# Kernel optimization log

Measured on AMD Instinct MI355X. Metric: run time of the kernel, lower is better.

## Reference

```python
import jax, jax.numpy as jnp
import numpy as np

B, N, M, DIN, H = 8, 2048, 2048, 512, 256
SCALE = float(np.sqrt(H))


def _lin_params(key, din, dout):
    kw, kb = jax.random.split(key)
    lim = 1.0 / np.sqrt(din)
    W = jax.random.uniform(kw, (din, dout), jnp.float32, -lim, lim)
    b = jax.random.uniform(kb, (dout,), jnp.float32, -lim, lim)
    return W, b


def setup_inputs() -> dict:
    key = jax.random.key(0)
    ks = jax.random.split(key, 16)
    inp = {
        "q_fp": jax.random.normal(ks[0], (B, N, DIN), jnp.float32),
        "v_ret": jax.random.normal(ks[1], (B, M, DIN), jnp.float32),
        "pi_star": jax.random.uniform(ks[2], (B, N, M), jnp.float32),
    }
    names = ["qs", "ks", "vs", "qe", "ke", "ve"]
    for i, nm in enumerate(names):
        W, b = _lin_params(ks[3 + i], DIN, H)
        inp[f"W{nm}"], inp[f"b{nm}"] = W, b
    inp["W1"], inp["b1"] = _lin_params(ks[10], 4 * H, H)
    inp["W2"], inp["b2"] = _lin_params(ks[11], H, H)
    inp["gamma"] = jnp.ones((1,), jnp.float32)
    inp["ew"] = jnp.array(1.0, jnp.float32)
    return inp


def _forward(q_fp, v_ret, pi_star, Wqs, bqs, Wks, bks, Wvs, bvs,
             Wqe, bqe, Wke, bke, Wve, bve, W1, b1, W2, b2, gamma, ew):
    q_struct = q_fp @ Wqs + bqs          # [B,N,H]
    k_struct = v_ret @ Wks + bks         # [B,M,H]
    v_struct = v_ret @ Wvs + bvs
    q_elec = q_fp @ Wqe + bqe
    k_elec = v_ret @ Wke + bke
    v_elec = v_ret @ Wve + bve

    structural_logits = jnp.einsum("bnh,bmh->bnm", q_struct, k_struct) / SCALE

    # cdist(p=2) via the quadratic expansion, clamped for numeric safety
    q2 = jnp.sum(q_elec * q_elec, -1, keepdims=True)          # [B,N,1]
    k2 = jnp.sum(k_elec * k_elec, -1, keepdims=True)          # [B,M,1]
    d2 = q2 + jnp.swapaxes(k2, -2, -1) - 2.0 * jnp.einsum("bnh,bmh->bnm", q_elec, k_elec)
    electronic_distance = jnp.sqrt(jnp.maximum(d2, 1e-12))    # [B,N,M]
    electronic_scale = jnp.maximum(
        electronic_distance.mean(axis=(-2, -1), keepdims=True), 1e-4)
    electronic_logits = -(electronic_distance / electronic_scale)

    pi_mask = gamma * jnp.log(jnp.maximum(pi_star, 1e-9))
    final_logits = structural_logits + ew * electronic_logits + pi_mask
    attn = jax.nn.softmax(final_logits, axis=-1)              # [B,N,M]

    ctx_s = jnp.einsum("bnm,bmh->bnh", attn, v_struct)
    ctx_e = jnp.einsum("bnm,bmh->bnh", attn, v_elec)
    fused = jnp.concatenate([ctx_s, ctx_e, ctx_s - ctx_e, ctx_s * ctx_e], axis=-1)
    h = jax.nn.silu(fused @ W1 + b1)
    return h @ W2 + b2


def reference(q_fp, v_ret, pi_star, Wqs, bqs, Wks, bks, Wvs, bvs,
              Wqe, bqe, Wke, bke, Wve, bve, W1, b1, W2, b2, gamma, ew):
    return _forward(q_fp, v_ret, pi_star, Wqs, bqs, Wks, bks, Wvs, bvs,
                    Wqe, bqe, Wke, bke, Wve, bve, W1, b1, W2, b2, gamma, ew)
```

## Files before the change

### kernel.cpp

```cpp
#include <hip/hip_runtime.h>

#define Bsz 8
#define Nq  2048
#define Mk  2048
#define BKt 32
#define BUFE (128 * BKt)

typedef __attribute__((ext_vector_type(8))) short   short8;
typedef __attribute__((ext_vector_type(4))) float   floatx4;

__device__ __forceinline__ unsigned short f2bf(float f) {
  union { float f; unsigned u; } x; x.f = f;
  unsigned r = x.u + 0x7fffu + ((x.u >> 16) & 1u);
  return (unsigned short)(r >> 16);
}
__device__ __forceinline__ float bf2f(unsigned short s) {
  union { unsigned u; float f; } x; x.u = ((unsigned)s) << 16;
  return x.f;
}

__device__ __forceinline__ void gload16(const unsigned short* g, unsigned short* l) {
  __builtin_amdgcn_global_load_lds(
      (const __attribute__((address_space(1))) void*)g,
      (__attribute__((address_space(3))) void*)l, 16, 0, 0);
}

__device__ __forceinline__ void gemm_core8_nt(
    const unsigned short* __restrict__ A, int lda,
    const unsigned short* __restrict__ B, int ldb,
    int K, unsigned short* ldsA, unsigned short* ldsB,
    floatx4 (&acc)[4][2])
{
  const int tid  = threadIdx.x;
  const int lane = tid & 63;
  const int wid  = tid >> 6;
  const int wm   = wid & 1;
  const int wn   = wid >> 1;
  const int fr   = lane & 15;
  const int fk   = (lane >> 4) << 3;
  const int lr   = lane >> 2;
  const int lc   = (lane & 3) << 3;
  const int r0   = wid << 4;

  const unsigned short* gA = A + (size_t)(r0 + lr) * lda + lc;
  const unsigned short* gB = B + (size_t)(r0 + lr) * ldb + lc;
  unsigned short* lA = ldsA + r0 * BKt;
  unsigned short* lB = ldsB + r0 * BKt;
  const unsigned short* fa = ldsA + (wm * 64 + fr) * BKt + fk;
  const unsigned short* fb = ldsB + (wn * 32 + fr) * BKt + fk;

  gload16(gA, lA); gA += BKt;
  gload16(gB, lB); gB += BKt;
  __syncthreads();

  int cur = 0;
  for (int k0 = 0; k0 < K; k0 += BKt) {
    const int nxt = cur ^ 1;
    if (k0 + BKt < K) {
      gload16(gA, lA + nxt * BUFE); gA += BKt;
      gload16(gB, lB + nxt * BUFE); gB += BKt;
    }
    const unsigned short* fac = fa + cur * BUFE;
    const unsigned short* fbc = fb + cur * BUFE;
    short8 af[4], bfr[2];
#pragma unroll
    for (int i = 0; i < 4; i++) af[i]  = *(const short8*)(fac + i * 16 * BKt);
#pragma unroll
    for (int j = 0; j < 2; j++) bfr[j] = *(const short8*)(fbc + j * 16 * BKt);
#pragma unroll
    for (int i = 0; i < 4; i++)
#pragma unroll
      for (int j = 0; j < 2; j++)
        acc[i][j] = __builtin_amdgcn_mfma_f32_16x16x32_bf16(af[i], bfr[j], acc[i][j], 0, 0, 0);
    __syncthreads();
    cur = nxt;
  }
}

#define EPILOGUE_VARS \
  const int lane = threadIdx.x & 63; \
  const int wid  = threadIdx.x >> 6; \
  const int wm   = wid & 1; \
  const int wn   = wid >> 1; \
  const int r4   = (lane >> 4) * 4;  \
  const int cn   = lane & 15; \
  (void)wid;

template<int MODE>
__global__ __launch_bounds__(512, 4) void k_gemm_bias(
    const unsigned short* __restrict__ A, const unsigned short* __restrict__ Bw,
    const float* __restrict__ bias, void* __restrict__ Cout, int Ncols, int K)
{
  __shared__ alignas(16) unsigned short ldsA[2 * BUFE];
  __shared__ alignas(16) unsigned short ldsB[2 * BUFE];
  floatx4 acc[4][2];
#pragma unroll
  for (int i = 0; i < 4; i++)
#pragma unroll
    for (int j = 0; j < 2; j++)
#pragma unroll
      for (int t = 0; t < 4; t++) acc[i][j][t] = 0.f;

  const unsigned short* Ab = A + (size_t)blockIdx.x * 128 * K;
  const unsigned short* Bb = Bw + (size_t)blockIdx.y * 128 * K;
  gemm_core8_nt(Ab, K, Bb, K, K, ldsA, ldsB, acc);

  EPILOGUE_VARS
#pragma unroll
  for (int i = 0; i < 4; i++) {
#pragma unroll
    for (int j = 0; j < 2; j++) {
      int gc = blockIdx.y * 128 + wn * 32 + j * 16 + cn;
      float bv = bias[gc];
#pragma unroll
      for (int r = 0; r < 4; r++) {
        int gr = blockIdx.x * 128 + wm * 64 + i * 16 + r4 + r;
        float v = acc[i][j][r] + bv;
        if constexpr (MODE == 1) v = v / (1.f + __expf(-v));
        if constexpr (MODE == 2)
          ((float*)Cout)[(size_t)gr * Ncols + gc] = v;
        else
          ((unsigned short*)Cout)[(size_t)gr * Ncols + gc] = f2bf(v);
      }
    }
  }
}

__global__ __launch_bounds__(512) void k_cast(
    const float* __restrict__ src, unsigned short* __restrict__ dst, int n8)
{
  for (int i = blockIdx.x * 512 + threadIdx.x; i < n8; i += gridDim.x * 512) {
    const float4 f0 = *(const float4*)(src + (size_t)i * 8);
    const float4 f1 = *(const float4*)(src + (size_t)i * 8 + 4);
    uint4 p;
    p.x = f2bf(f0.x) | ((unsigned)f2bf(f0.y) << 16);
    p.y = f2bf(f0.z) | ((unsigned)f2bf(f0.w) << 16);
    p.z = f2bf(f1.x) | ((unsigned)f2bf(f1.y) << 16);
    p.w = f2bf(f1.z) | ((unsigned)f2bf(f1.w) << 16);
    *(uint4*)(dst + (size_t)i * 8) = p;
  }
}

__global__ __launch_bounds__(512, 4) void k_sd(
    const unsigned short* __restrict__ Xq, const unsigned short* __restrict__ Xk,
    const float* __restrict__ q2, const float* __restrict__ k2,
    int b0, float* __restrict__ dsum, unsigned* __restrict__ sd)
{
  __shared__ alignas(16) unsigned short ldsAs[2 * BUFE];
  __shared__ alignas(16) unsigned short ldsAe[2 * BUFE];
  __shared__ alignas(16) unsigned short ldsBs[2 * BUFE];
  __shared__ alignas(16) unsigned short ldsBe[2 * BUFE];
  floatx4 accS[4][2], accE[4][2];
#pragma unroll
  for (int i = 0; i < 4; i++)
#pragma unroll
    for (int j = 0; j < 2; j++)
#pragma unroll
      for (int t = 0; t < 4; t++) { accS[i][j][t] = 0.f; accE[i][j][t] = 0.f; }

  const int z = blockIdx.z;
  const int b = b0 + z;

  const int tid  = threadIdx.x;
  const int lane = tid & 63;
  const int wid  = tid >> 6;
  const int wm   = wid & 1;
  const int wn   = wid >> 1;
  const int fr   = lane & 15;
  const int fk   = (lane >> 4) << 3;
  const int lr   = lane >> 2;
  const int lc   = (lane & 3) << 3;
  const int r0   = wid << 4;

  const unsigned short* gAs = Xq + ((size_t)(b * Nq) + blockIdx.x * 128 + r0 + lr) * 512 + lc;
  const unsigned short* gAe = gAs + 256;
  const unsigned short* gBs = Xk + ((size_t)(b * Mk) + blockIdx.y * 128 + r0 + lr) * 1024 + lc;
  const unsigned short* gBe = gBs + 512;
  unsigned short* lAs = ldsAs + r0 * BKt;
  unsigned short* lAe = ldsAe + r0 * BKt;
  unsigned short* lBs = ldsBs + r0 * BKt;
  unsigned short* lBe = ldsBe + r0 * BKt;
  const unsigned short* fas = ldsAs + (wm * 64 + fr) * BKt + fk;
  const unsigned short* fae = ldsAe + (wm * 64 + fr) * BKt + fk;
  const unsigned short* fbs = ldsBs + (wn * 32 + fr) * BKt + fk;
  const unsigned short* fbe = ldsBe + (wn * 32 + fr) * BKt + fk;

  gload16(gAs, lAs); gAs += BKt;
  gload16(gAe, lAe); gAe += BKt;
  gload16(gBs, lBs); gBs += BKt;
  gload16(gBe, lBe); gBe += BKt;
  __syncthreads();

  int cur = 0;
  for (int k0 = 0; k0 < 256; k0 += BKt) {
    const int nxt = cur ^ 1;
    if (k0 + BKt < 256) {
      gload16(gAs, lAs + nxt * BUFE); gAs += BKt;
      gload16(gAe, lAe + nxt * BUFE); gAe += BKt;
      gload16(gBs, lBs + nxt * BUFE); gBs += BKt;
      gload16(gBe, lBe + nxt * BUFE); gBe += BKt;
    }
    {
      short8 af[4], bfr[2];
      const unsigned short* fac = fas + cur * BUFE;
      const unsigned short* fbc = fbs + cur * BUFE;
#pragma unroll
      for (int i = 0; i < 4; i++) af[i]  = *(const short8*)(fac + i * 16 * BKt);
#pragma unroll
      for (int j = 0; j < 2; j++) bfr[j] = *(const short8*)(fbc + j * 16 * BKt);
#pragma unroll
      for (int i = 0; i < 4; i++)
#pragma unroll
        for (int j = 0; j < 2; j++)
          accS[i][j] = __builtin_amdgcn_mfma_f32_16x16x32_bf16(af[i], bfr[j], accS[i][j], 0, 0, 0);
    }
    {
      short8 af[4], bfr[2];
      const unsigned short* fac = fae + cur * BUFE;
      const unsigned short* fbc = fbe + cur * BUFE;
#pragma unroll
      for (int i = 0; i < 4; i++) af[i]  = *(const short8*)(fac + i * 16 * BKt);
#pragma unroll
      for (int j = 0; j < 2; j++) bfr[j] = *(const short8*)(fbc + j * 16 * BKt);
#pragma unroll
      for (int i = 0; i < 4; i++)
#pragma unroll
        for (int j = 0; j < 2; j++)
          accE[i][j] = __builtin_amdgcn_mfma_f32_16x16x32_bf16(af[i], bfr[j], accE[i][j], 0, 0, 0);
    }
    __syncthreads();
    cur = nxt;
  }

  const int r4 = (lane >> 4) * 4;
  const int cn = lane & 15;
  const int colT = blockIdx.y * 128 + wn * 32;
  const float kk0 = k2[b * Mk + colT + cn];
  const float kk1 = k2[b * Mk + colT + 16 + cn];

  float lsum = 0.f;
#pragma unroll
  for (int i = 0; i < 4; i++) {
#pragma unroll
    for (int r = 0; r < 4; r++) {
      const int n = blockIdx.x * 128 + wm * 64 + i * 16 + r4 + r;
      const float qq = q2[b * Nq + n];
      unsigned* srow = sd + (size_t)(z * Nq + n) * Mk;
#pragma unroll
      for (int j = 0; j < 2; j++) {
        const int m = colT + j * 16 + cn;
        float d = sqrtf(fmaxf(qq + (j ? kk1 : kk0) - 2.f * accE[i][j][r], 1e-12f));
        lsum += d;
        srow[m] = (unsigned)f2bf(accS[i][j][r] * 0.0625f)
                | ((unsigned)f2bf(d) << 16);
      }
    }
  }
#pragma unroll
  for (int o = 32; o; o >>= 1) lsum += __shfl_down(lsum, o);
  __syncthreads();
  float* red = (float*)ldsAs;
  if (lane == 0) red[wid] = lsum;
  __syncthreads();
  if (threadIdx.x == 0) {
    float s = 0.f;
#pragma unroll
    for (int t = 0; t < 8; t++) s += red[t];
    atomicAdd(dsum + b, s);
  }
}

__global__ __launch_bounds__(256) void k_softmax(
    const unsigned* __restrict__ sd, const float* __restrict__ pi,
    const float* __restrict__ dsum, const float* __restrict__ gamma_p,
    const float* __restrict__ ew_p, int b0,
    unsigned short* __restrict__ attn, float* __restrict__ rowsum)
{
  const int wid  = threadIdx.x >> 6;
  const int lane = threadIdx.x & 63;
  const int rl   = blockIdx.x * 4 + wid;
  const int b    = b0 + (rl >> 11);
  const int n    = rl & 2047;

  const float scale = fmaxf(dsum[b] * (1.f / (2048.f * 2048.f)), 1e-4f);
  const float einv  = ew_p[0] / scale;
  const float gv    = gamma_p[0];
  const bool  g1    = (gv == 1.0f);

  const unsigned*  sp = sd  + (size_t)rl * Mk;
  const float*     pp = pi  + ((size_t)b * Nq + n) * Mk;
  unsigned short*  ap = attn + ((size_t)b * Nq + n) * Mk;

  float rs = 0.f;
  for (int it = 0; it < 8; ++it) {
    const int c = it * 256 + lane * 4;
    const uint4  sv = *(const uint4*)(sp + c);
    const float4 pv = *(const float4*)(pp + c);
    const unsigned uu[4]  = {sv.x, sv.y, sv.z, sv.w};
    const float    pp4[4] = {pv.x, pv.y, pv.z, pv.w};
    float e[4];
#pragma unroll
    for (int t = 0; t < 4; ++t) {
      union { unsigned u; float f; } cs, cd;
      cs.u = uu[t] << 16;
      cd.u = uu[t] & 0xffff0000u;
      float p  = fmaxf(pp4[t], 1e-9f);
      float pf = g1 ? p : __expf(gv * __logf(p));
      e[t] = __expf(cs.f - einv * cd.f) * pf;
      rs += e[t];
    }
    uint2 st;
    st.x = (unsigned)f2bf(e[0]) | ((unsigned)f2bf(e[1]) << 16);
    st.y = (unsigned)f2bf(e[2]) | ((unsigned)f2bf(e[3]) << 16);
    *(uint2*)(ap + c) = st;
  }
#pragma unroll
  for (int o = 32; o; o >>= 1) rs += __shfl_down(rs, o);
  if (lane == 0) rowsum[b * Nq + n] = rs;
}

__global__ __launch_bounds__(512, 4) void k_pv(
    const unsigned short* __restrict__ At, const unsigned short* __restrict__ VT,
    const float* __restrict__ rowsum, unsigned short* __restrict__ ctx)
{
  __shared__ alignas(16) unsigned short ldsA[2 * BUFE];
  __shared__ alignas(16) unsigned short ldsB[2 * BUFE];
  floatx4 acc[4][2];
#pragma unroll
  for (int i = 0; i < 4; i++)
#pragma unroll
    for (int j = 0; j < 2; j++)
#pragma unroll
      for (int t = 0; t < 4; t++) acc[i][j][t] = 0.f;

  const int l  = blockIdx.x;
  const int lg = ((l & 7) << 3) | (l >> 3);
  const int tx = lg >> 2;
  const int ty = lg & 3;
  const int b  = blockIdx.z;
  const unsigned short* Ab = At + ((size_t)b * Nq + tx * 128) * (size_t)Mk;
  const unsigned short* Bb = VT + ((size_t)b * 512 + ty * 128) * (size_t)Mk;
  gemm_core8_nt(Ab, Mk, Bb, Mk, Mk, ldsA, ldsB, acc);

  EPILOGUE_VARS
  const int rowbase = b * Nq + tx * 128 + wm * 64;
#pragma unroll
  for (int i = 0; i < 4; i++) {
    float rinv[4];
#pragma unroll
    for (int r = 0; r < 4; r++)
      rinv[r] = 1.f / rowsum[rowbase + i * 16 + r4 + r];
#pragma unroll
    for (int j = 0; j < 2; j++) {
      int gc = ty * 128 + wn * 32 + j * 16 + cn;
#pragma unroll
      for (int r = 0; r < 4; r++) {
        int gr = tx * 128 + wm * 64 + i * 16 + r4 + r;
        ctx[((size_t)b * Nq + gr) * 512 + gc] = f2bf(acc[i][j][r] * rinv[r]);
      }
    }
  }
}

__global__ void k_prep_w(
    const float* __restrict__ Wqs, const float* __restrict__ Wqe,
    const float* __restrict__ Wks, const float* __restrict__ Wvs,
    const float* __restrict__ Wke, const float* __restrict__ Wve,
    const float* __restrict__ W1,  const float* __restrict__ W2,
    const float* __restrict__ bqs, const float* __restrict__ bqe,
    const float* __restrict__ bks, const float* __restrict__ bvs,
    const float* __restrict__ bke, const float* __restrict__ bve,
    unsigned short* __restrict__ WqT, unsigned short* __restrict__ WkT,
    unsigned short* __restrict__ W1T, unsigned short* __restrict__ W2T,
    float* __restrict__ bq, float* __restrict__ bk, float* __restrict__ dsum)
{
  int gid = blockIdx.x * 256 + threadIdx.x;
  int idx = gid;
  if (idx < 512 * 512) {
    int j = idx >> 9, k = idx & 511;
    float v = (j < 256) ? Wqs[k * 256 + j] : Wqe[k * 256 + (j - 256)];
    WqT[idx] = f2bf(v);
  } else if ((idx -= 512 * 512) < 1024 * 512) {
    int j = idx >> 9, k = idx & 511;
    int s = j >> 8, jj = j & 255;
    const float* Wp = (s == 0) ? Wks : (s == 1) ? Wvs : (s == 2) ? Wke : Wve;
    WkT[idx] = f2bf(Wp[k * 256 + jj]);
  } else if ((idx -= 1024 * 512) < 256 * 1024) {
    int j = idx >> 10, k = idx & 1023;
    W1T[idx] = f2bf(W1[k * 256 + j]);
  } else if ((idx -= 256 * 1024) < 256 * 256) {
    int j = idx >> 8, k = idx & 255;
    W2T[idx] = f2bf(W2[k * 256 + j]);
  }
  if (gid < 512)  bq[gid] = (gid < 256) ? bqs[gid] : bqe[gid - 256];
  if (gid < 1024) bk[gid] = (gid < 256) ? bks[gid]
                    : (gid < 512) ? bvs[gid - 256]
                    : (gid < 768) ? bke[gid - 512] : bve[gid - 768];
  if (gid < 8) dsum[gid] = 0.f;
}

__global__ __launch_bounds__(256) void k_rowsq(
    const unsigned short* __restrict__ X, int stride, int colOff, float* __restrict__ out)
{
  int row = blockIdx.x * 4 + (threadIdx.x >> 6);
  int lane = threadIdx.x & 63;
  const unsigned short* p = X + (size_t)row * stride + colOff + lane * 4;
  uint2 u = *(const uint2*)p;
  float a0 = bf2f((unsigned short)(u.x & 0xffff));
  float a1 = bf2f((unsigned short)(u.x >> 16));
  float a2 = bf2f((unsigned short)(u.y & 0xffff));
  float a3 = bf2f((unsigned short)(u.y >> 16));
  float s = a0 * a0 + a1 * a1 + a2 * a2 + a3 * a3;
#pragma unroll
  for (int o = 32; o; o >>= 1) s += __shfl_down(s, o);
  if (lane == 0) out[row] = s;
}

__global__ void k_trans_vt(const unsigned short* __restrict__ Xk, unsigned short* __restrict__ VT) {
  __shared__ unsigned short t[32][33];
  const int b = blockIdx.z;
  const int m0 = blockIdx.x * 32, j0 = blockIdx.y * 32;
  const int tx = threadIdx.x, ty = threadIdx.y;
#pragma unroll
  for (int i = 0; i < 4; i++) {
    int m = m0 + ty + i * 8;
    int j = j0 + tx;
    int c = (j < 256) ? (256 + j) : (512 + j);
    t[ty + i * 8][tx] = Xk[((size_t)b * Mk + m) * 1024 + c];
  }
  __syncthreads();
#pragma unroll
  for (int i = 0; i < 4; i++) {
    int j = j0 + ty + i * 8;
    int m = m0 + tx;
    VT[((size_t)b * 512 + j) * Mk + m] = t[tx][ty + i * 8];
  }
}

__global__ void k_fused(const unsigned short* __restrict__ ctx, unsigned short* __restrict__ fused) {
  int idx = blockIdx.x * 256 + threadIdx.x;
  int bn = idx >> 8;
  int j = idx & 255;
  float cs = bf2f(ctx[(size_t)bn * 512 + j]);
  float ce = bf2f(ctx[(size_t)bn * 512 + 256 + j]);
  size_t o = (size_t)bn * 1024 + j;
  fused[o]       = f2bf(cs);
  fused[o + 256] = f2bf(ce);
  fused[o + 512] = f2bf(cs - ce);
  fused[o + 768] = f2bf(cs * ce);
}

extern "C" void kernel_launch(void* const* d_in, const int* in_sizes, int n_in,
                              void* d_out, int out_size, void* d_ws, size_t ws_size,
                              hipStream_t stream) {
  (void)in_sizes; (void)n_in; (void)out_size; (void)ws_size;
  const float* q_fp  = (const float*)d_in[0];
  const float* v_ret = (const float*)d_in[1];
  const float* pi    = (const float*)d_in[2];
  const float* Wqs = (const float*)d_in[3];  const float* bqs = (const float*)d_in[4];
  const float* Wks = (const float*)d_in[5];  const float* bks = (const float*)d_in[6];
  const float* Wvs = (const float*)d_in[7];  const float* bvs = (const float*)d_in[8];
  const float* Wqe = (const float*)d_in[9];  const float* bqe = (const float*)d_in[10];
  const float* Wke = (const float*)d_in[11]; const float* bke = (const float*)d_in[12];
  const float* Wve = (const float*)d_in[13]; const float* bve = (const float*)d_in[14];
  const float* W1  = (const float*)d_in[15]; const float* b1  = (const float*)d_in[16];
  const float* W2  = (const float*)d_in[17]; const float* b2  = (const float*)d_in[18];
  const float* gamma = (const float*)d_in[19];
  const float* ew    = (const float*)d_in[20];

  char* w = (char*)d_ws;
  unsigned short* WqT = (unsigned short*)(w + 0);
  unsigned short* WkT = (unsigned short*)(w + 524288);
  unsigned short* W1T = (unsigned short*)(w + 1572864);
  unsigned short* W2T = (unsigned short*)(w + 2097152);
  float* bq   = (float*)(w + 2228224);
  float* bk   = (float*)(w + 2230272);
  float* q2   = (float*)(w + 2234368);
  float* k2   = (float*)(w + 2299904);
  float* dsum = (float*)(w + 2365440);
  unsigned short* ctx  = (unsigned short*)(w + 2365696);
  unsigned short* hbuf = (unsigned short*)(w + 19142912);
  unsigned short* Xq = (unsigned short*)(w + 35920128);
  unsigned short* Xk = (unsigned short*)(w + 52697344);
  unsigned short* VT = (unsigned short*)(w + 86251776);
  unsigned short* attn = (unsigned short*)(w + 103028992);
  unsigned short* fused = attn;
  unsigned short* castQ = (unsigned short*)(w + 103028992);
  unsigned short* castK = (unsigned short*)(w + 103028992 + 16777216);
  unsigned* sdbuf = (unsigned*)(w + 2365696);
  float* rowsum = (float*)d_out;

  k_prep_w<<<4352, 256, 0, stream>>>(Wqs, Wqe, Wks, Wvs, Wke, Wve, W1, W2,
                                     bqs, bqe, bks, bvs, bke, bve,
                                     WqT, WkT, W1T, W2T, bq, bk, dsum);
  k_cast<<<2048, 512, 0, stream>>>(q_fp,  castQ, (16384 * 512) / 8);
  k_cast<<<2048, 512, 0, stream>>>(v_ret, castK, (16384 * 512) / 8);
  k_gemm_bias<0><<<dim3(128, 4), 512, 0, stream>>>(castQ, WqT, bq, Xq, 512, 512);
  k_gemm_bias<0><<<dim3(128, 8), 512, 0, stream>>>(castK, WkT, bk, Xk, 1024, 512);
  k_rowsq<<<4096, 256, 0, stream>>>(Xq, 512, 256, q2);
  k_rowsq<<<4096, 256, 0, stream>>>(Xk, 1024, 512, k2);
  for (int c = 0; c < 4; ++c) {
    k_sd<<<dim3(16, 16, 2), 512, 0, stream>>>(Xq, Xk, q2, k2, 2 * c, dsum, sdbuf);
    k_softmax<<<1024, 256, 0, stream>>>(sdbuf, pi, dsum, gamma, ew, 2 * c,
                                        attn, rowsum);
  }
  k_trans_vt<<<dim3(64, 16, 8), dim3(32, 8), 0, stream>>>(Xk, VT);
  k_pv<<<dim3(64, 1, 8), 512, 0, stream>>>(attn, VT, rowsum, ctx);
  k_fused<<<16384, 256, 0, stream>>>(ctx, fused);
  k_gemm_bias<1><<<dim3(128, 2), 512, 0, stream>>>(fused, W1T, b1, hbuf, 256, 1024);
  k_gemm_bias<2><<<dim3(128, 2), 512, 0, stream>>>(hbuf, W2T, b2, d_out, 256, 256);
}
```

Baseline: 559.4 us.

## Fuse row-norms into projection GEMMs and fused-concat into PV epilogue

Folds the squared-norm reductions into the projection GEMM epilogues via shuffles and atomics, merges the two cast kernels, and has the PV kernel pair struct/elec column tiles per block so it writes the concatenated fused tensor directly. This removes several small launches and the intermediate ctx round trip through memory. In exchange it adds atomics with nondeterministic summation order, zero-init in prep, an LDS staging pass, and a workspace reshuffle where attn, hbuf and cast buffers alias.

```diff
diff --git a/kernel.cpp b/kernel.cpp
--- a/kernel.cpp
+++ b/kernel.cpp
@@ -126,18 +126,78 @@
   }
 }
 
-__global__ __launch_bounds__(512) void k_cast(
-    const float* __restrict__ src, unsigned short* __restrict__ dst, int n8)
-{
-  for (int i = blockIdx.x * 512 + threadIdx.x; i < n8; i += gridDim.x * 512) {
-    const float4 f0 = *(const float4*)(src + (size_t)i * 8);
-    const float4 f1 = *(const float4*)(src + (size_t)i * 8 + 4);
+__global__ __launch_bounds__(512, 4) void k_proj_sq(
+    const unsigned short* __restrict__ A, const unsigned short* __restrict__ Bw,
+    const float* __restrict__ bias, unsigned short* __restrict__ Cout,
+    int Ncols, int K, float* __restrict__ sq, int elecOff)
+{
+  __shared__ alignas(16) unsigned short ldsA[2 * BUFE];
+  __shared__ alignas(16) unsigned short ldsB[2 * BUFE];
+  floatx4 acc[4][2];
+#pragma unroll
+  for (int i = 0; i < 4; i++)
+#pragma unroll
+    for (int j = 0; j < 2; j++)
+#pragma unroll
+      for (int t = 0; t < 4; t++) acc[i][j][t] = 0.f;
+
+  const unsigned short* Ab = A + (size_t)blockIdx.x * 128 * K;
+  const unsigned short* Bb = Bw + (size_t)blockIdx.y * 128 * K;
+  gemm_core8_nt(Ab, K, Bb, K, K, ldsA, ldsB, acc);
+
+  EPILOGUE_VARS
+  const int c0 = blockIdx.y * 128;
+  const bool insq = (c0 >= elecOff) && (c0 < elecOff + 256);
+#pragma unroll
+  for (int i = 0; i < 4; i++) {
+    float s4[4] = {0.f, 0.f, 0.f, 0.f};
+#pragma unroll
+    for (int j = 0; j < 2; j++) {
+      int gc = c0 + wn * 32 + j * 16 + cn;
+      float bv = bias[gc];
+#pragma unroll
+      for (int r = 0; r < 4; r++) {
+        int gr = blockIdx.x * 128 + wm * 64 + i * 16 + r4 + r;
+        float v = acc[i][j][r] + bv;
+        unsigned short us = f2bf(v);
+        Cout[(size_t)gr * Ncols + gc] = us;
+        if (insq) { float vr = bf2f(us); s4[r] += vr * vr; }
+      }
+    }
+    if (insq) {
+#pragma unroll
+      for (int r = 0; r < 4; r++) {
+        s4[r] += __shfl_xor(s4[r], 1);
+        s4[r] += __shfl_xor(s4[r], 2);
+        s4[r] += __shfl_xor(s4[r], 4);
+        s4[r] += __shfl_xor(s4[r], 8);
+      }
+      if (cn == 0) {
+#pragma unroll
+        for (int r = 0; r < 4; r++)
+          atomicAdd(sq + blockIdx.x * 128 + wm * 64 + i * 16 + r4 + r, s4[r]);
+      }
+    }
+  }
+}
+
+__global__ __launch_bounds__(512) void k_cast2(
+    const float* __restrict__ a, const float* __restrict__ b,
+    unsigned short* __restrict__ da, unsigned short* __restrict__ db, int n8each)
+{
+  const int total = 2 * n8each;
+  for (int i = blockIdx.x * 512 + threadIdx.x; i < total; i += gridDim.x * 512) {
+    const float* s; unsigned short* d; int k;
+    if (i < n8each) { s = a; d = da; k = i; }
+    else            { s = b; d = db; k = i - n8each; }
+    const float4 f0 = *(const float4*)(s + (size_t)k * 8);
+    const float4 f1 = *(const float4*)(s + (size_t)k * 8 + 4);
     uint4 p;
     p.x = f2bf(f0.x) | ((unsigned)f2bf(f0.y) << 16);
     p.y = f2bf(f0.z) | ((unsigned)f2bf(f0.w) << 16);
     p.z = f2bf(f1.x) | ((unsigned)f2bf(f1.y) << 16);
     p.w = f2bf(f1.z) | ((unsigned)f2bf(f1.w) << 16);
-    *(uint4*)(dst + (size_t)i * 8) = p;
+    *(uint4*)(d + (size_t)k * 8) = p;
   }
 }
 
@@ -321,10 +381,11 @@
 
 __global__ __launch_bounds__(512, 4) void k_pv(
     const unsigned short* __restrict__ At, const unsigned short* __restrict__ VT,
-    const float* __restrict__ rowsum, unsigned short* __restrict__ ctx)
-{
-  __shared__ alignas(16) unsigned short ldsA[2 * BUFE];
-  __shared__ alignas(16) unsigned short ldsB[2 * BUFE];
+    const float* __restrict__ rowsum, unsigned short* __restrict__ fused)
+{
+  __shared__ alignas(16) unsigned short smem[4 * BUFE];
+  unsigned short* ldsA = smem;
+  unsigned short* ldsB = smem + 2 * BUFE;
   floatx4 acc[4][2];
 #pragma unroll
   for (int i = 0; i < 4; i++)
@@ -338,12 +399,16 @@
   const int tx = lg >> 2;
   const int ty = lg & 3;
   const int b  = blockIdx.z;
-  const unsigned short* Ab = At + ((size_t)b * Nq + tx * 128) * (size_t)Mk;
-  const unsigned short* Bb = VT + ((size_t)b * 512 + ty * 128) * (size_t)Mk;
-  gemm_core8_nt(Ab, Mk, Bb, Mk, Mk, ldsA, ldsB, acc);
+  const unsigned short* Ab  = At + ((size_t)b * Nq + tx * 128) * (size_t)Mk;
+  const unsigned short* Bb0 = VT + ((size_t)b * 512 + ty * 64) * (size_t)Mk;
+  const unsigned short* Bb1 = VT + ((size_t)b * 512 + 256 + ty * 64) * (size_t)Mk;
+  const int wid0 = threadIdx.x >> 6;
+  const unsigned short* Beff = (wid0 < 4) ? Bb0 : (Bb1 - (size_t)64 * Mk);
+  gemm_core8_nt(Ab, Mk, Beff, Mk, Mk, ldsA, ldsB, acc);
 
   EPILOGUE_VARS
   const int rowbase = b * Nq + tx * 128 + wm * 64;
+  unsigned short (*ctile)[128] = (unsigned short(*)[128])smem;
 #pragma unroll
   for (int i = 0; i < 4; i++) {
     float rinv[4];
@@ -352,13 +417,26 @@
       rinv[r] = 1.f / rowsum[rowbase + i * 16 + r4 + r];
 #pragma unroll
     for (int j = 0; j < 2; j++) {
-      int gc = ty * 128 + wn * 32 + j * 16 + cn;
-#pragma unroll
-      for (int r = 0; r < 4; r++) {
-        int gr = tx * 128 + wm * 64 + i * 16 + r4 + r;
-        ctx[((size_t)b * Nq + gr) * 512 + gc] = f2bf(acc[i][j][r] * rinv[r]);
-      }
-    }
+      const int lc2 = wn * 32 + j * 16 + cn;
+#pragma unroll
+      for (int r = 0; r < 4; r++)
+        ctile[wm * 64 + i * 16 + r4 + r][lc2] = f2bf(acc[i][j][r] * rinv[r]);
+    }
+  }
+  __syncthreads();
+  const int tid = threadIdx.x;
+  for (int p = tid; p < 128 * 64; p += 512) {
+    const int row = p >> 6;
+    const int c   = p & 63;
+    const unsigned short us = ctile[row][c];
+    const unsigned short ue = ctile[row][64 + c];
+    const float cs = bf2f(us);
+    const float ce = bf2f(ue);
+    unsigned short* out = fused + ((size_t)(b * Nq) + tx * 128 + row) * 1024 + ty * 64 + c;
+    out[0]   = us;
+    out[256] = ue;
+    out[512] = f2bf(cs - ce);
+    out[768] = f2bf(cs * ce);
   }
 }
 
@@ -372,7 +450,8 @@
     const float* __restrict__ bke, const float* __restrict__ bve,
     unsigned short* __restrict__ WqT, unsigned short* __restrict__ WkT,
     unsigned short* __restrict__ W1T, unsigned short* __restrict__ W2T,
-    float* __restrict__ bq, float* __restrict__ bk, float* __restrict__ dsum)
+    float* __restrict__ bq, float* __restrict__ bk, float* __restrict__ dsum,
+    float* __restrict__ q2z, float* __restrict__ k2z)
 {
   int gid = blockIdx.x * 256 + threadIdx.x;
   int idx = gid;
@@ -397,23 +476,8 @@
                     : (gid < 512) ? bvs[gid - 256]
                     : (gid < 768) ? bke[gid - 512] : bve[gid - 768];
   if (gid < 8) dsum[gid] = 0.f;
-}
-
-__global__ __launch_bounds__(256) void k_rowsq(
-    const unsigned short* __restrict__ X, int stride, int colOff, float* __restrict__ out)
-{
-  int row = blockIdx.x * 4 + (threadIdx.x >> 6);
-  int lane = threadIdx.x & 63;
-  const unsigned short* p = X + (size_t)row * stride + colOff + lane * 4;
-  uint2 u = *(const uint2*)p;
-  float a0 = bf2f((unsigned short)(u.x & 0xffff));
-  float a1 = bf2f((unsigned short)(u.x >> 16));
-  float a2 = bf2f((unsigned short)(u.y & 0xffff));
-  float a3 = bf2f((unsigned short)(u.y >> 16));
-  float s = a0 * a0 + a1 * a1 + a2 * a2 + a3 * a3;
-#pragma unroll
-  for (int o = 32; o; o >>= 1) s += __shfl_down(s, o);
-  if (lane == 0) out[row] = s;
+  if (gid < 16384) q2z[gid] = 0.f;
+  else if (gid < 32768) k2z[gid - 16384] = 0.f;
 }
 
 __global__ void k_trans_vt(const unsigned short* __restrict__ Xk, unsigned short* __restrict__ VT) {
@@ -435,19 +499,6 @@
     int m = m0 + tx;
     VT[((size_t)b * 512 + j) * Mk + m] = t[tx][ty + i * 8];
   }
-}
-
-__global__ void k_fused(const unsigned short* __restrict__ ctx, unsigned short* __restrict__ fused) {
-  int idx = blockIdx.x * 256 + threadIdx.x;
-  int bn = idx >> 8;
-  int j = idx & 255;
-  float cs = bf2f(ctx[(size_t)bn * 512 + j]);
-  float ce = bf2f(ctx[(size_t)bn * 512 + 256 + j]);
-  size_t o = (size_t)bn * 1024 + j;
-  fused[o]       = f2bf(cs);
-  fused[o + 256] = f2bf(ce);
-  fused[o + 512] = f2bf(cs - ce);
-  fused[o + 768] = f2bf(cs * ce);
 }
 
 extern "C" void kernel_launch(void* const* d_in, const int* in_sizes, int n_in,
@@ -478,35 +529,30 @@
   float* q2   = (float*)(w + 2234368);
   float* k2   = (float*)(w + 2299904);
   float* dsum = (float*)(w + 2365440);
-  unsigned short* ctx  = (unsigned short*)(w + 2365696);
-  unsigned short* hbuf = (unsigned short*)(w + 19142912);
+  unsigned* sdbuf = (unsigned*)(w + 2365696);
+  unsigned short* fused = (unsigned short*)(w + 2365696);
   unsigned short* Xq = (unsigned short*)(w + 35920128);
   unsigned short* Xk = (unsigned short*)(w + 52697344);
   unsigned short* VT = (unsigned short*)(w + 86251776);
-  unsigned short* attn = (unsigned short*)(w + 103028992);
-  unsigned short* fused = attn;
   unsigned short* castQ = (unsigned short*)(w + 103028992);
   unsigned short* castK = (unsigned short*)(w + 103028992 + 16777216);
-  unsigned* sdbuf = (unsigned*)(w + 2365696);
+  unsigned short* attn  = (unsigned short*)(w + 103028992);
+  unsigned short* hbuf  = (unsigned short*)(w + 103028992);
   float* rowsum = (float*)d_out;
 
   k_prep_w<<<4352, 256, 0, stream>>>(Wqs, Wqe, Wks, Wvs, Wke, Wve, W1, W2,
                                      bqs, bqe, bks, bvs, bke, bve,
-                                     WqT, WkT, W1T, W2T, bq, bk, dsum);
-  k_cast<<<2048, 512, 0, stream>>>(q_fp,  castQ, (16384 * 512) / 8);
-  k_cast<<<2048, 512, 0, stream>>>(v_ret, castK, (16384 * 512) / 8);
-  k_gemm_bias<0><<<dim3(128, 4), 512, 0, stream>>>(castQ, WqT, bq, Xq, 512, 512);
-  k_gemm_bias<0><<<dim3(128, 8), 512, 0, stream>>>(castK, WkT, bk, Xk, 1024, 512);
-  k_rowsq<<<4096, 256, 0, stream>>>(Xq, 512, 256, q2);
-  k_rowsq<<<4096, 256, 0, stream>>>(Xk, 1024, 512, k2);
+                                     WqT, WkT, W1T, W2T, bq, bk, dsum, q2, k2);
+  k_cast2<<<2048, 512, 0, stream>>>(q_fp, v_ret, castQ, castK, (16384 * 512) / 8);
+  k_proj_sq<<<dim3(128, 4), 512, 0, stream>>>(castQ, WqT, bq, Xq, 512, 512, q2, 256);
+  k_proj_sq<<<dim3(128, 8), 512, 0, stream>>>(castK, WkT, bk, Xk, 1024, 512, k2, 512);
   for (int c = 0; c < 4; ++c) {
     k_sd<<<dim3(16, 16, 2), 512, 0, stream>>>(Xq, Xk, q2, k2, 2 * c, dsum, sdbuf);
     k_softmax<<<1024, 256, 0, stream>>>(sdbuf, pi, dsum, gamma, ew, 2 * c,
                                         attn, rowsum);
   }
   k_trans_vt<<<dim3(64, 16, 8), dim3(32, 8), 0, stream>>>(Xk, VT);
-  k_pv<<<dim3(64, 1, 8), 512, 0, stream>>>(attn, VT, rowsum, ctx);
-  k_fused<<<16384, 256, 0, stream>>>(ctx, fused);
+  k_pv<<<dim3(64, 1, 8), 512, 0, stream>>>(attn, VT, rowsum, fused);
   k_gemm_bias<1><<<dim3(128, 2), 512, 0, stream>>>(fused, W1T, b1, hbuf, 256, 1024);
   k_gemm_bias<2><<<dim3(128, 2), 512, 0, stream>>>(hbuf, W2T, b2, d_out, 256, 256);
 }
```

Result: no change. 550.8 us (-1.5%).
